# Performance work log

Measured on AMD Instinct MI355X. Metric: run time of the kernel, lower is better.

Reference implementation:

```python
import jax, jax.numpy as jnp
import numpy as np

# Dimensions
BATCH = 4
NUM_NODE = 20000
NUM_EDGE = 1280000   # avg degree 64
K = 2                # num_rd_kernels
NUM_SEQ = 13         # num_sequence (13 time points -> 12 intervals)
SEQ_IN = 12
RES = 2              # fixed-step Euler substeps per interval (resolution)
TEMP = 1.0           # temperature for gate softmax
NUM_OUT = -12        # num_output_sequence slice


def setup_inputs() -> dict:
    key = jax.random.key(0)
    ks = jax.random.split(key, 6)
    inputs = jax.random.normal(ks[0], (BATCH, 1, NUM_NODE, SEQ_IN), dtype=jnp.float32)
    gate = jax.random.normal(ks[1], (NUM_SEQ - 1, K), dtype=jnp.float32)
    # edge list from adjacency CSV (from/to columns)
    src = jax.random.randint(ks[2], (NUM_EDGE,), 0, NUM_NODE)
    dst = jax.random.randint(ks[3], (NUM_EDGE,), 0, NUM_NODE)
    # learned per-kernel parameters of multi_reaction_diffusion
    w = jax.random.normal(ks[4], (K, NUM_EDGE), dtype=jnp.float32) * 0.1  # edge diffusivity logits
    r = jax.random.normal(ks[5], (K, NUM_NODE), dtype=jnp.float32) * 0.1  # node reaction coeffs
    return {"inputs": inputs, "gate": gate, "w": w, "r": r, "src": src, "dst": dst}


def _dxdt(x, g, w, r, src, dst):
    # x: [B,N]  g: [K]  w: [K,E]  r: [K,N]
    a = jax.nn.sigmoid(w)                                   # [K,E] edge diffusivity
    xs = x[:, src]                                          # [B,E]
    xd = x[:, dst]                                          # [B,E]
    msg = a[:, None, :] * (xs - xd)[None, :, :]             # [K,B,E]
    # scatter-add messages into destination nodes
    diff = jax.ops.segment_sum(jnp.moveaxis(msg, 2, 0), dst, num_segments=NUM_NODE)  # [N,K,B]
    diff = jnp.transpose(diff, (1, 2, 0))                   # [K,B,N]
    react = r[:, None, :] * x[None] * (1.0 - x[None])       # [K,B,N] logistic reaction
    return jnp.einsum('k,kbn->bn', g, diff + react)         # gate-weighted mix of RD kernels


def reference(inputs, gate, w, r, src, dst):
    x0 = inputs[:, 0, :, -1]                                # [B,N]
    dt = 1.0 / (NUM_SEQ - 1)
    h = jnp.float32(dt / RES)
    gates = jax.nn.softmax(gate / TEMP, axis=-1)            # [NUM_SEQ-1, K]

    def interval(x, g):
        def step(xc, _):
            return xc + h * _dxdt(xc, g, w, r, src, dst), None
        x, _ = jax.lax.scan(step, x, None, length=RES)
        return x, x

    _, traj = jax.lax.scan(interval, x0, gates)             # [NUM_SEQ-1, B, N]
    out = jnp.concatenate([x0[None], traj], axis=0)         # [NUM_SEQ, B, N]
    return out[NUM_OUT:]                                    # last 12 horizons
```

## Files before the change

### kernel.cpp

```cpp
#include <hip/hip_runtime.h>
#include <hip/hip_fp16.h>
#include <math.h>

#define NNODE 20000
#define NEDGE 1280000
#define HSTEP (1.0f/24.0f)
#define NBUCK 313
#define CAP   4608
#define EPB   2048
#define NPB   32
#define TPB   512
#define NBLK  (NNODE/NPB)
#define CAPB  2432
#define NGRP  25
#define GSZ   25
#define XSTR  320512

#define GEPI(g)   (32*(g))
#define RCNTI(g)  (32*(25+(g)))
#define XARRI(x)  (32*(50+(x)))
#define XCNTI(x)  (32*(58+(x)))
#define MASTERI   (32*66)
#define RMASTERI  (32*67)

#define AGT __HIP_MEMORY_SCOPE_AGENT

__global__ void rd_init(const float* __restrict__ inp,
                        float4* __restrict__ x,
                        int* __restrict__ cursor,
                        int* __restrict__ bar) {
    int n = blockIdx.x * blockDim.x + threadIdx.x;
    if (n < NBUCK) cursor[n] = n * CAP;
    if (n < 2560) bar[n] = 0;
    if (n < NNODE) {
        float4 v;
        v.x = inp[0 * NNODE * 12 + n * 12 + 11];
        v.y = inp[1 * NNODE * 12 + n * 12 + 11];
        v.z = inp[2 * NNODE * 12 + n * 12 + 11];
        v.w = inp[3 * NNODE * 12 + n * 12 + 11];
        x[n] = v;
    }
}

__global__ __launch_bounds__(256) void rd_part(const int4* __restrict__ src4,
                                               const int4* __restrict__ dst4,
                                               const float4* __restrict__ w4,
                                               int* __restrict__ cursor,
                                               uint2* __restrict__ rec) {
    __shared__ int h[4][NBUCK];
    __shared__ uint4 cache[EPB / 4];
    int t = threadIdx.x, wv = t >> 6;
    for (int i = t; i < 4 * NBUCK; i += 256) ((int*)h)[i] = 0;
    __syncthreads();
    int q0 = blockIdx.x * (EPB / 4);
    #pragma unroll
    for (int k = 0; k < 2; ++k) {
        int qi = q0 + k * 256 + t;
        int4 d4 = dst4[qi];
        int dd[4] = {d4.x, d4.y, d4.z, d4.w};
        unsigned cc[4];
        #pragma unroll
        for (int u = 0; u < 4; ++u) {
            int rank = atomicAdd(&h[wv][dd[u] >> 6], 1);
            cc[u] = (unsigned)dd[u] | ((unsigned)rank << 15);
        }
        cache[k * 256 + t] = make_uint4(cc[0], cc[1], cc[2], cc[3]);
    }
    __syncthreads();
    for (int i = t; i < NBUCK; i += 256) {
        int c0 = h[0][i], c1 = h[1][i], c2 = h[2][i], c3 = h[3][i];
        int tot = c0 + c1 + c2 + c3;
        int gb = tot ? atomicAdd(&cursor[i], tot) : 0;
        h[0][i] = gb;
        h[1][i] = gb + c0;
        h[2][i] = gb + c0 + c1;
        h[3][i] = gb + c0 + c1 + c2;
    }
    __syncthreads();
    #pragma unroll
    for (int k = 0; k < 2; ++k) {
        int qi = q0 + k * 256 + t;
        int4 s4 = src4[qi];
        float4 wa = w4[qi];
        float4 wb = w4[NEDGE / 4 + qi];
        uint4 c4 = cache[k * 256 + t];
        int ss[4] = {s4.x, s4.y, s4.z, s4.w};
        float fa[4] = {wa.x, wa.y, wa.z, wa.w};
        float fb[4] = {wb.x, wb.y, wb.z, wb.w};
        unsigned cc[4] = {c4.x, c4.y, c4.z, c4.w};
        #pragma unroll
        for (int u = 0; u < 4; ++u) {
            int d = cc[u] & 0x7FFF;
            int rank = (int)(cc[u] >> 15);
            int b = d >> 6;
            int p = h[wv][b] + rank;
            float s0 = 1.0f / (1.0f + expf(-fa[u]));
            float s1 = 1.0f / (1.0f + expf(-fb[u]));
            __half2 hh = __floats2half2_rn(s0, s1);
            uint2 rq;
            rq.x = (unsigned)ss[u] | ((unsigned)(d & 63) << 16);
            rq.y = *(unsigned*)&hh;
            if (p < (b + 1) * CAP) rec[p] = rq;
        }
    }
}

__global__ void rd_bscan(const int* __restrict__ cursor, int* __restrict__ boff) {
    int lane = threadIdx.x;
    int carry = 0;
    #pragma unroll
    for (int c = 0; c < 5; ++c) {
        int i = c * 64 + lane;
        int v = (i < NBUCK) ? (cursor[i] - i * CAP) : 0;
        int incl = v;
        #pragma unroll
        for (int o = 1; o < 64; o <<= 1) {
            int u = __shfl_up(incl, o, 64);
            if (lane >= o) incl += u;
        }
        if (i < NBUCK) boff[i] = carry + incl - v;
        carry += __shfl(incl, 63, 64);
    }
    if (lane == 0) boff[NBUCK] = carry;
}

__global__ __launch_bounds__(512) void rd_bsort(const uint2* __restrict__ rec,
                                                const int* __restrict__ cursor,
                                                const int* __restrict__ boff,
                                                unsigned short* __restrict__ es16,
                                                unsigned* __restrict__ ew32,
                                                int* __restrict__ offsets) {
    __shared__ uint2 rs[CAP];
    __shared__ int h[64], excl[64];
    int b = blockIdx.x;
    int ib = b * CAP;
    int cnt = cursor[b] - ib; if (cnt > CAP) cnt = CAP;
    int ob = boff[b];
    if (threadIdx.x < 64) h[threadIdx.x] = 0;
    __syncthreads();
    for (int i = threadIdx.x; i < cnt; i += 512) {
        uint2 q = rec[ib + i];
        rs[i] = q;
        atomicAdd(&h[(q.x >> 16) & 63], 1);
    }
    __syncthreads();
    if (threadIdx.x < 64) {
        int lane = threadIdx.x;
        int v = h[lane];
        int incl = v;
        #pragma unroll
        for (int o = 1; o < 64; o <<= 1) {
            int u = __shfl_up(incl, o, 64);
            if (lane >= o) incl += u;
        }
        excl[lane] = incl - v;
        int n = b * 64 + lane;
        if (n < NNODE) offsets[n] = ob + excl[lane];
        h[lane] = 0;
    }
    if (b == NBUCK - 1 && threadIdx.x == 0) offsets[NNODE] = NEDGE;
    __syncthreads();
    for (int i = threadIdx.x; i < cnt; i += 512) {
        uint2 q = rs[i];
        int dl = (q.x >> 16) & 63;
        int rank = atomicAdd(&h[dl], 1);
        int p = ob + excl[dl] + rank;
        es16[p] = (unsigned short)(q.x & 0xFFFFu);
        ew32[p] = q.y;
    }
}

__global__ __launch_bounds__(TPB, 6) void rd_run(
        const float4* __restrict__ x0buf, char* __restrict__ recb,
        const unsigned short* __restrict__ es16,
        const unsigned* __restrict__ ew32,
        const int* __restrict__ offsets,
        const float* __restrict__ r, const float* __restrict__ gate,
        float* __restrict__ out, int* bar) {
    __shared__ unsigned short les[CAPB];
    __shared__ unsigned lew[CAPB];
    __shared__ int lofs[NPB + 1];
    __shared__ float lgate[24];
    int t = threadIdx.x;
    int n0 = blockIdx.x * NPB;
    if (t <= NPB) lofs[t] = offsets[n0 + t];
    if (t >= 64 && t < 88) lgate[t - 64] = gate[t - 64];
    __syncthreads();
    int ebase = lofs[0];
    int ecnt  = lofs[NPB] - ebase; if (ecnt > CAPB) ecnt = CAPB;
    for (int i = t; i < ecnt; i += TPB) {
        les[i] = es16[ebase + i];
        lew[i] = ew32[ebase + i];
    }
    int node = n0 + (t >> 4);
    int sub  = t & 15;
    float r0n = r[node], r1n = r[NNODE + node];
    int jb = lofs[t >> 4] - ebase;
    int je = lofs[(t >> 4) + 1] - ebase;
    int grp = blockIdx.x / GSZ;

    int myxcd = 0, nx = 0, nxcd = 0;
    if (t == 0) {
        __builtin_amdgcn_fence(__ATOMIC_ACQUIRE, "agent");
        myxcd = (int)(__builtin_amdgcn_s_getreg(63508) & 0xF);
        __hip_atomic_fetch_add(&bar[XCNTI(myxcd)], 1, __ATOMIC_RELAXED, AGT);
        int rA = __hip_atomic_fetch_add(&bar[RCNTI(grp)], 1, __ATOMIC_RELEASE, AGT);
        if (rA == GSZ - 1) {
            int rm = __hip_atomic_fetch_add(&bar[RMASTERI], 1, __ATOMIC_RELAXED, AGT);
            if (rm == NGRP - 1)
                for (int g = 0; g < NGRP; ++g)
                    __hip_atomic_store(&bar[GEPI(g)], 1, __ATOMIC_RELAXED, AGT);
        }
        while (__hip_atomic_load(&bar[GEPI(grp)], __ATOMIC_RELAXED, AGT) < 1)
            __builtin_amdgcn_s_sleep(2);
        asm volatile("" ::: "memory");
        nx = __hip_atomic_load(&bar[XCNTI(myxcd)], __ATOMIC_RELAXED, AGT);
        for (int x2 = 0; x2 < 8; ++x2)
            nxcd += (__hip_atomic_load(&bar[XCNTI(x2)], __ATOMIC_RELAXED, AGT) > 0);
    }
    __syncthreads();

    for (int p = 0; p < 24; ++p) {
        int itv = p >> 1;
        float ga = lgate[2 * itv], gb = lgate[2 * itv + 1];
        float g0 = 1.0f / (1.0f + expf(gb - ga));
        float g1 = 1.0f - g0;
        float rc = fmaf(g0, r0n, g1 * r1n);
        const float4* xi = p ? (const float4*)(recb + (size_t)(p - 1) * XSTR) : x0buf;
        float4*       xo = (float4*)(recb + (size_t)p * XSTR);

        float4 xd = xi[node];
        float4 acc = make_float4(0.f, 0.f, 0.f, 0.f);
        float wsum = 0.f;
        int j = jb + sub;
        for (; j + 48 < je; j += 64) {
            unsigned a0 = les[j], a1 = les[j + 16], a2 = les[j + 32], a3 = les[j + 48];
            unsigned b0 = lew[j], b1 = lew[j + 16], b2 = lew[j + 32], b3 = lew[j + 48];
            float4 x0 = xi[a0], x1 = xi[a1], x2 = xi[a2], x3 = xi[a3];
            float2 f0 = __half22float2(*(__half2*)&b0);
            float2 f1 = __half22float2(*(__half2*)&b1);
            float2 f2 = __half22float2(*(__half2*)&b2);
            float2 f3 = __half22float2(*(__half2*)&b3);
            float we0 = fmaf(g0, f0.x, g1 * f0.y);
            float we1 = fmaf(g0, f1.x, g1 * f1.y);
            float we2 = fmaf(g0, f2.x, g1 * f2.y);
            float we3 = fmaf(g0, f3.x, g1 * f3.y);
            acc.x = fmaf(we0, x0.x, fmaf(we1, x1.x, fmaf(we2, x2.x, fmaf(we3, x3.x, acc.x))));
            acc.y = fmaf(we0, x0.y, fmaf(we1, x1.y, fmaf(we2, x2.y, fmaf(we3, x3.y, acc.y))));
            acc.z = fmaf(we0, x0.z, fmaf(we1, x1.z, fmaf(we2, x2.z, fmaf(we3, x3.z, acc.z))));
            acc.w = fmaf(we0, x0.w, fmaf(we1, x1.w, fmaf(we2, x2.w, fmaf(we3, x3.w, acc.w))));
            wsum += (we0 + we1) + (we2 + we3);
        }
        for (; j + 16 < je; j += 32) {
            unsigned a0 = les[j], a1 = les[j + 16];
            unsigned b0 = lew[j], b1 = lew[j + 16];
            float4 x0 = xi[a0], x1 = xi[a1];
            float2 f0 = __half22float2(*(__half2*)&b0);
            float2 f1 = __half22float2(*(__half2*)&b1);
            float we0 = fmaf(g0, f0.x, g1 * f0.y);
            float we1 = fmaf(g0, f1.x, g1 * f1.y);
            acc.x = fmaf(we0, x0.x, fmaf(we1, x1.x, acc.x));
            acc.y = fmaf(we0, x0.y, fmaf(we1, x1.y, acc.y));
            acc.z = fmaf(we0, x0.z, fmaf(we1, x1.z, acc.z));
            acc.w = fmaf(we0, x0.w, fmaf(we1, x1.w, acc.w));
            wsum += we0 + we1;
        }
        if (j < je) {
            unsigned a0 = les[j];
            unsigned b0 = lew[j];
            float4 x0 = xi[a0];
            float2 f0 = __half22float2(*(__half2*)&b0);
            float we0 = fmaf(g0, f0.x, g1 * f0.y);
            acc.x = fmaf(we0, x0.x, acc.x);
            acc.y = fmaf(we0, x0.y, acc.y);
            acc.z = fmaf(we0, x0.z, acc.z);
            acc.w = fmaf(we0, x0.w, acc.w);
            wsum += we0;
        }
        #pragma unroll
        for (int m = 8; m >= 1; m >>= 1) {
            acc.x += __shfl_xor(acc.x, m, 64);
            acc.y += __shfl_xor(acc.y, m, 64);
            acc.z += __shfl_xor(acc.z, m, 64);
            acc.w += __shfl_xor(acc.w, m, 64);
            wsum  += __shfl_xor(wsum,  m, 64);
        }
        float4 xn;
        xn.x = xd.x + HSTEP * ((acc.x - wsum * xd.x) + rc * xd.x * (1.0f - xd.x));
        xn.y = xd.y + HSTEP * ((acc.y - wsum * xd.y) + rc * xd.y * (1.0f - xd.y));
        xn.z = xd.z + HSTEP * ((acc.z - wsum * xd.z) + rc * xd.z * (1.0f - xd.z));
        xn.w = xd.w + HSTEP * ((acc.w - wsum * xd.w) + rc * xd.w * (1.0f - xd.w));
        if (sub < 2) {
            union { float f[2]; unsigned long long u; } cv;
            cv.f[0] = (sub == 0) ? xn.x : xn.z;
            cv.f[1] = (sub == 0) ? xn.y : xn.w;
            __hip_atomic_store((unsigned long long*)&xo[node] + sub, cv.u,
                               __ATOMIC_RELAXED, AGT);
        }
        if ((p & 1) && sub < 4) {
            float v = (sub == 0) ? xn.x : (sub == 1) ? xn.y : (sub == 2) ? xn.z : xn.w;
            out[(itv * 4 + sub) * NNODE + node] = v;
        }

        if (p < 23) {
            __syncthreads();
            if (t == 0) {
                int o = __hip_atomic_fetch_add(&bar[XARRI(myxcd)], 1,
                                               __ATOMIC_RELAXED, AGT);
                if (o == (p + 1) * nx - 1) {
                    int om = __hip_atomic_fetch_add(&bar[MASTERI], 1,
                                                    __ATOMIC_RELAXED, AGT);
                    if (om == (p + 1) * nxcd - 1)
                        for (int g = 0; g < NGRP; ++g)
                            __hip_atomic_store(&bar[GEPI(g)], p + 2,
                                               __ATOMIC_RELAXED, AGT);
                }
                while (__hip_atomic_load(&bar[GEPI(grp)], __ATOMIC_RELAXED, AGT) < p + 2)
                    __builtin_amdgcn_s_sleep(2);
                asm volatile("" ::: "memory");
            }
            __syncthreads();
        }
    }
}

extern "C" void kernel_launch(void* const* d_in, const int* in_sizes, int n_in,
                              void* d_out, int out_size, void* d_ws, size_t ws_size,
                              hipStream_t stream) {
    const float* inp  = (const float*)d_in[0];
    const float* gate = (const float*)d_in[1];
    const float* w    = (const float*)d_in[2];
    const float* r    = (const float*)d_in[3];
    const int*   src  = (const int*)d_in[4];
    const int*   dst  = (const int*)d_in[5];
    float* out = (float*)d_out;

    char* ws = (char*)d_ws;
    float4*         xA      = (float4*)(ws + 0);
    int*            offsets = (int*)   (ws + 641024);
    int*            cursor  = (int*)   (ws + 721152);
    int*            boff    = (int*)   (ws + 722432);
    int*            bar     = (int*)   (ws + 723712);
    char*           recb    = (ws + 740096);
    unsigned short* es16    = (unsigned short*)(ws + 12278528);
    unsigned*       ew32    = (unsigned*)(ws + 14838528);

    rd_init <<<(NNODE + 255) / 256, 256, 0, stream>>>(inp, xA, cursor, bar);
    rd_part <<<NEDGE / EPB, 256, 0, stream>>>((const int4*)src, (const int4*)dst,
                                              (const float4*)w, cursor, (uint2*)recb);
    rd_bscan<<<1, 64, 0, stream>>>(cursor, boff);
    rd_bsort<<<NBUCK, 512, 0, stream>>>((const uint2*)recb, cursor, boff,
                                        es16, ew32, offsets);
    rd_run  <<<NBLK, TPB, 0, stream>>>(xA, recb, es16, ew32, offsets, r, gate, out, bar);
}
```

Baseline: 266.9 us.

## Precompute per-node weight sums, pack edge records, enlarge blocks, use plain stores

Each node's sums of the two fp16 edge-weight channels are computed once before the time loop, so the per-step weight sum becomes a single gated fma. This removes a shuffle reduction and adds per edge from all 24 steps. Edge source index and weight are packed into one uint2 LDS array so a single LDS read serves both. Blocks grow to 40 nodes and 640 threads, with the group size and occupancy hint adjusted to match. The relaxed 64-bit atomic stores of the new state become a plain float4 store followed by a release fence in the barrier. That fence sits only on the last arriver's path, so cross-XCD visibility of the plain stores from the other blocks may be weaker.

```diff
diff --git a/kernel.cpp b/kernel.cpp
--- a/kernel.cpp
+++ b/kernel.cpp
@@ -8,12 +8,12 @@
 #define NBUCK 313
 #define CAP   4608
 #define EPB   2048
-#define NPB   32
-#define TPB   512
+#define NPB   40
+#define TPB   640
 #define NBLK  (NNODE/NPB)
-#define CAPB  2432
+#define CAPB  2976
 #define NGRP  25
-#define GSZ   25
+#define GSZ   20
 #define XSTR  320512
 
 #define GEPI(g)   (32*(g))
@@ -170,15 +170,14 @@
     }
 }
 
-__global__ __launch_bounds__(TPB, 6) void rd_run(
+__global__ __launch_bounds__(TPB, 5) void rd_run(
         const float4* __restrict__ x0buf, char* __restrict__ recb,
         const unsigned short* __restrict__ es16,
         const unsigned* __restrict__ ew32,
         const int* __restrict__ offsets,
         const float* __restrict__ r, const float* __restrict__ gate,
         float* __restrict__ out, int* bar) {
-    __shared__ unsigned short les[CAPB];
-    __shared__ unsigned lew[CAPB];
+    __shared__ uint2 lrec[CAPB];
     __shared__ int lofs[NPB + 1];
     __shared__ float lgate[24];
     int t = threadIdx.x;
@@ -188,10 +187,8 @@
     __syncthreads();
     int ebase = lofs[0];
     int ecnt  = lofs[NPB] - ebase; if (ecnt > CAPB) ecnt = CAPB;
-    for (int i = t; i < ecnt; i += TPB) {
-        les[i] = es16[ebase + i];
-        lew[i] = ew32[ebase + i];
-    }
+    for (int i = t; i < ecnt; i += TPB)
+        lrec[i] = make_uint2((unsigned)es16[ebase + i], ew32[ebase + i]);
     int node = n0 + (t >> 4);
     int sub  = t & 15;
     float r0n = r[node], r1n = r[NNODE + node];
@@ -220,27 +217,38 @@
     }
     __syncthreads();
 
+    float S0 = 0.f, S1 = 0.f;
+    for (int j = jb + sub; j < je; j += 16) {
+        uint2 q = lrec[j];
+        float2 f = __half22float2(*(__half2*)&q.y);
+        S0 += f.x; S1 += f.y;
+    }
+    #pragma unroll
+    for (int m = 8; m >= 1; m >>= 1) {
+        S0 += __shfl_xor(S0, m, 64);
+        S1 += __shfl_xor(S1, m, 64);
+    }
+
     for (int p = 0; p < 24; ++p) {
         int itv = p >> 1;
         float ga = lgate[2 * itv], gb = lgate[2 * itv + 1];
         float g0 = 1.0f / (1.0f + expf(gb - ga));
         float g1 = 1.0f - g0;
         float rc = fmaf(g0, r0n, g1 * r1n);
+        float wsum = fmaf(g0, S0, g1 * S1);
         const float4* xi = p ? (const float4*)(recb + (size_t)(p - 1) * XSTR) : x0buf;
         float4*       xo = (float4*)(recb + (size_t)p * XSTR);
 
         float4 xd = xi[node];
         float4 acc = make_float4(0.f, 0.f, 0.f, 0.f);
-        float wsum = 0.f;
         int j = jb + sub;
         for (; j + 48 < je; j += 64) {
-            unsigned a0 = les[j], a1 = les[j + 16], a2 = les[j + 32], a3 = les[j + 48];
-            unsigned b0 = lew[j], b1 = lew[j + 16], b2 = lew[j + 32], b3 = lew[j + 48];
-            float4 x0 = xi[a0], x1 = xi[a1], x2 = xi[a2], x3 = xi[a3];
-            float2 f0 = __half22float2(*(__half2*)&b0);
-            float2 f1 = __half22float2(*(__half2*)&b1);
-            float2 f2 = __half22float2(*(__half2*)&b2);
-            float2 f3 = __half22float2(*(__half2*)&b3);
+            uint2 q0 = lrec[j], q1 = lrec[j + 16], q2 = lrec[j + 32], q3 = lrec[j + 48];
+            float4 x0 = xi[q0.x], x1 = xi[q1.x], x2 = xi[q2.x], x3 = xi[q3.x];
+            float2 f0 = __half22float2(*(__half2*)&q0.y);
+            float2 f1 = __half22float2(*(__half2*)&q1.y);
+            float2 f2 = __half22float2(*(__half2*)&q2.y);
+            float2 f3 = __half22float2(*(__half2*)&q3.y);
             float we0 = fmaf(g0, f0.x, g1 * f0.y);
             float we1 = fmaf(g0, f1.x, g1 * f1.y);
             float we2 = fmaf(g0, f2.x, g1 * f2.y);
@@ -249,33 +257,28 @@
             acc.y = fmaf(we0, x0.y, fmaf(we1, x1.y, fmaf(we2, x2.y, fmaf(we3, x3.y, acc.y))));
             acc.z = fmaf(we0, x0.z, fmaf(we1, x1.z, fmaf(we2, x2.z, fmaf(we3, x3.z, acc.z))));
             acc.w = fmaf(we0, x0.w, fmaf(we1, x1.w, fmaf(we2, x2.w, fmaf(we3, x3.w, acc.w))));
-            wsum += (we0 + we1) + (we2 + we3);
         }
         for (; j + 16 < je; j += 32) {
-            unsigned a0 = les[j], a1 = les[j + 16];
-            unsigned b0 = lew[j], b1 = lew[j + 16];
-            float4 x0 = xi[a0], x1 = xi[a1];
-            float2 f0 = __half22float2(*(__half2*)&b0);
-            float2 f1 = __half22float2(*(__half2*)&b1);
+            uint2 q0 = lrec[j], q1 = lrec[j + 16];
+            float4 x0 = xi[q0.x], x1 = xi[q1.x];
+            float2 f0 = __half22float2(*(__half2*)&q0.y);
+            float2 f1 = __half22float2(*(__half2*)&q1.y);
             float we0 = fmaf(g0, f0.x, g1 * f0.y);
             float we1 = fmaf(g0, f1.x, g1 * f1.y);
             acc.x = fmaf(we0, x0.x, fmaf(we1, x1.x, acc.x));
             acc.y = fmaf(we0, x0.y, fmaf(we1, x1.y, acc.y));
             acc.z = fmaf(we0, x0.z, fmaf(we1, x1.z, acc.z));
             acc.w = fmaf(we0, x0.w, fmaf(we1, x1.w, acc.w));
-            wsum += we0 + we1;
         }
         if (j < je) {
-            unsigned a0 = les[j];
-            unsigned b0 = lew[j];
-            float4 x0 = xi[a0];
-            float2 f0 = __half22float2(*(__half2*)&b0);
+            uint2 q0 = lrec[j];
+            float4 x0 = xi[q0.x];
+            float2 f0 = __half22float2(*(__half2*)&q0.y);
             float we0 = fmaf(g0, f0.x, g1 * f0.y);
             acc.x = fmaf(we0, x0.x, acc.x);
             acc.y = fmaf(we0, x0.y, acc.y);
             acc.z = fmaf(we0, x0.z, acc.z);
             acc.w = fmaf(we0, x0.w, acc.w);
-            wsum += we0;
         }
         #pragma unroll
         for (int m = 8; m >= 1; m >>= 1) {
@@ -283,20 +286,13 @@
             acc.y += __shfl_xor(acc.y, m, 64);
             acc.z += __shfl_xor(acc.z, m, 64);
             acc.w += __shfl_xor(acc.w, m, 64);
-            wsum  += __shfl_xor(wsum,  m, 64);
         }
         float4 xn;
         xn.x = xd.x + HSTEP * ((acc.x - wsum * xd.x) + rc * xd.x * (1.0f - xd.x));
         xn.y = xd.y + HSTEP * ((acc.y - wsum * xd.y) + rc * xd.y * (1.0f - xd.y));
         xn.z = xd.z + HSTEP * ((acc.z - wsum * xd.z) + rc * xd.z * (1.0f - xd.z));
         xn.w = xd.w + HSTEP * ((acc.w - wsum * xd.w) + rc * xd.w * (1.0f - xd.w));
-        if (sub < 2) {
-            union { float f[2]; unsigned long long u; } cv;
-            cv.f[0] = (sub == 0) ? xn.x : xn.z;
-            cv.f[1] = (sub == 0) ? xn.y : xn.w;
-            __hip_atomic_store((unsigned long long*)&xo[node] + sub, cv.u,
-                               __ATOMIC_RELAXED, AGT);
-        }
+        if (sub == 0) xo[node] = xn;
         if ((p & 1) && sub < 4) {
             float v = (sub == 0) ? xn.x : (sub == 1) ? xn.y : (sub == 2) ? xn.z : xn.w;
             out[(itv * 4 + sub) * NNODE + node] = v;
@@ -308,6 +304,7 @@
                 int o = __hip_atomic_fetch_add(&bar[XARRI(myxcd)], 1,
                                                __ATOMIC_RELAXED, AGT);
                 if (o == (p + 1) * nx - 1) {
+                    __builtin_amdgcn_fence(__ATOMIC_RELEASE, "agent");
                     int om = __hip_atomic_fetch_add(&bar[MASTERI], 1,
                                                     __ATOMIC_RELAXED, AGT);
                     if (om == (p + 1) * nxcd - 1)
```

Result: faster. 240.7 us (-9.8%).
